# Kernel tuning notes

Measured on AMD Instinct MI355X. Metric: run time of the kernel, lower is better.

The kernel has to match this reference:

```python
import jax, jax.numpy as jnp
import numpy as np

EMBED_DIM = 128
BATCH = 8
SEQ = 2048


def setup_inputs() -> dict:
    key = jax.random.key(0)
    k1, k2, k3 = jax.random.split(key, 3)
    inputs = jax.random.normal(k1, (BATCH, SEQ, EMBED_DIM), dtype=jnp.float32)
    rotation_params = jax.random.normal(k2, (EMBED_DIM * 3,), dtype=jnp.float32)
    entangle_params = jax.random.normal(k3, (EMBED_DIM,), dtype=jnp.float32)
    return {"inputs": inputs, "rotation_params": rotation_params, "entangle_params": entangle_params}


def reference(inputs, rotation_params, entangle_params):
    d = inputs.shape[-1]
    rot = rotation_params.reshape(d, 3)          # [d, 3]
    ent = entangle_params.reshape(d, 1)          # [d, 1]
    query = inputs @ rot                         # [B, S, 3]
    key = inputs @ ent                           # [B, S, 1]
    # scores: [B, S, S], softmax over last axis
    logits = jnp.einsum('bsk,btk->bst', query, key) / jnp.sqrt(jnp.float32(d))
    scores = jax.nn.softmax(logits, axis=-1)
    return jnp.einsum('bst,btd->bsd', scores, inputs)  # [B, S, d]
```

## Files before the change

kernel.cpp:

```cpp
#include <hip/hip_runtime.h>
#include <cstddef>
#include <cstdint>

#define SS 2048
#define DD 128
#define NB 8

typedef _Float16 half8 __attribute__((ext_vector_type(8)));
typedef __attribute__((ext_vector_type(16))) float f32x16;

#define WS_A2   0
#define WS_KV   (NB*SS*4)
#define WS_XF   (2*NB*SS*4)
#define BATCH_B (SS*DD*2)
#define WS_NEED (size_t)(WS_XF + (size_t)NB*BATCH_B)
#define WS_KMX  (WS_XF)
#define WS_KMN  (WS_XF + 128)


__global__ __launch_bounds__(256) void prep(
    const float* __restrict__ X, const float* __restrict__ rotp,
    const float* __restrict__ entp, uint8_t* __restrict__ ws, int do_x) {
  __shared__ __align__(16) uint8_t lbuf[128 * 80];
  const int blk = blockIdx.x;
  const int b = blk & 7;
  const int rc = blk >> 3;
  const int tid = threadIdx.x;
  const int d4 = (tid & 31) * 4;
  float* a2out = (float*)(ws + WS_A2);
  float* kout = (float*)(ws + WS_KV);

  const float4 f0 = *reinterpret_cast<const float4*>(rotp + d4 * 3);
  const float4 f1 = *reinterpret_cast<const float4*>(rotp + d4 * 3 + 4);
  const float4 f2 = *reinterpret_cast<const float4*>(rotp + d4 * 3 + 8);
  const float rs0 = f0.x + f0.y + f0.z;
  const float rs1 = f0.w + f1.x + f1.y;
  const float rs2 = f1.z + f1.w + f2.x;
  const float rs3 = f2.y + f2.z + f2.w;
  const float4 e4 = *reinterpret_cast<const float4*>(entp + d4);

#pragma unroll
  for (int rnd = 0; rnd < 4; ++rnd) {
    const int t31 = rnd * 8 + (tid >> 5);
    const int tg = rc * 32 + t31;
    const float4 xv =
        *reinterpret_cast<const float4*>(X + ((size_t)b * SS + tg) * DD + d4);
    float av = xv.x * rs0 + xv.y * rs1 + xv.z * rs2 + xv.w * rs3;
    float kv = xv.x * e4.x + xv.y * e4.y + xv.z * e4.z + xv.w * e4.w;
#pragma unroll
    for (int off = 16; off > 0; off >>= 1) {
      av += __shfl_xor(av, off, 64);
      kv += __shfl_xor(kv, off, 64);
    }
    if ((tid & 31) == 0) {
      a2out[b * SS + tg] = av * (0.08838834764831845f * 1.4426950408889634f);
      kout[b * SS + tg] = kv;
    }
    if (do_x) {
      const float vv[4] = {xv.x, xv.y, xv.z, xv.w};
#pragma unroll
      for (int i = 0; i < 4; ++i)
        *reinterpret_cast<_Float16*>(lbuf + (d4 + i) * 80 + t31 * 2) =
            (_Float16)vv[i];
    }
  }

  if (do_x) {
    __syncthreads();
    const int T = rc >> 2;
    const int wfb = (rc & 3) * 2;
    uint8_t* outb = ws + WS_XF + (size_t)b * BATCH_B + (T * 8 + wfb) * 4096;
    const int nt = tid >> 6;
    const int lane = tid & 63;
    const int hh = lane >> 5;
    const int d = nt * 32 + (lane & 31);
#pragma unroll
    for (int wfl = 0; wfl < 2; ++wfl) {
      const half8 v = *reinterpret_cast<const half8*>(
          lbuf + d * 80 + (wfl * 16 + hh * 8) * 2);
      *reinterpret_cast<half8*>(outb + wfl * 4096 + nt * 1024 + lane * 16) = v;
    }
  }
}

__global__ __launch_bounds__(512, 2) void attn_mfma(
    const uint8_t* __restrict__ ws, float* __restrict__ out) {
  __shared__ float comb[2][64 * 128];
  __shared__ float dl[8 * 64];
  __shared__ float smx[8], smn[8];
  const int tid = threadIdx.x;
  const int w = tid >> 6;
  const int lane = tid & 63;
  const int lm = lane & 31;
  const int h = lane >> 5;
  const int blk = blockIdx.x;
  const int b = blk & 7;
  const int s0 = (blk >> 3) * 64;

  const float* a2 = (const float*)(ws + WS_A2) + b * SS;
  const float* kb = (const float*)(ws + WS_KV) + b * SS;
  const uint8_t* xf = ws + WS_XF + (size_t)b * BATCH_B;

  const float4 k4 = *reinterpret_cast<const float4*>(kb + tid * 4);
  float mx = fmaxf(fmaxf(k4.x, k4.y), fmaxf(k4.z, k4.w));
  float mn = fminf(fminf(k4.x, k4.y), fminf(k4.z, k4.w));
#pragma unroll
  for (int off = 32; off > 0; off >>= 1) {
    mx = fmaxf(mx, __shfl_xor(mx, off, 64));
    mn = fminf(mn, __shfl_xor(mn, off, 64));
  }
  if (lane == 0) { smx[w] = mx; smn[w] = mn; }
  const float ga0 = a2[s0 + lm];
  const float ga1 = a2[s0 + 32 + lm];
  __syncthreads();
  mx = smx[0]; mn = smn[0];
#pragma unroll
  for (int q = 1; q < 8; ++q) { mx = fmaxf(mx, smx[q]); mn = fminf(mn, smn[q]); }
  const float gm0 = fmaxf(ga0 * mx, ga0 * mn);
  const float gm1 = fmaxf(ga1 * mx, ga1 * mn);
  float gden0 = 0.0f, gden1 = 0.0f;

  f32x16 acc0[4], acc1[4];
#pragma unroll
  for (int nt = 0; nt < 4; ++nt)
#pragma unroll
    for (int r = 0; r < 16; ++r) { acc0[nt][r] = 0.0f; acc1[nt][r] = 0.0f; }

  const uint8_t* wb = xf + w * 4096 + lane * 16;
  half8 bf[4];
#pragma unroll
  for (int nt = 0; nt < 4; ++nt)
    bf[nt] = *reinterpret_cast<const half8*>(wb + nt * 1024);

  for (int T = 0; T < 16; ++T) {
    half8 bn[4];
    if (T < 15) {
      const uint8_t* nb_ = wb + (T + 1) * 32768;
#pragma unroll
      for (int nt = 0; nt < 4; ++nt)
        bn[nt] = *reinterpret_cast<const half8*>(nb_ + nt * 1024);
    }
    const float* kp = kb + T * 128 + w * 16 + h * 8;
    const float4 ka = *reinterpret_cast<const float4*>(kp);
    const float4 kc = *reinterpret_cast<const float4*>(kp + 4);
    const float kv8[8] = {ka.x, ka.y, ka.z, ka.w, kc.x, kc.y, kc.z, kc.w};
    half8 wa0, wa1;
#pragma unroll
    for (int j = 0; j < 8; ++j) {
      const float v0 = exp2f(fmaf(ga0, kv8[j], -gm0));
      const float v1 = exp2f(fmaf(ga1, kv8[j], -gm1));
      gden0 += v0; gden1 += v1;
      wa0[j] = (_Float16)v0;
      wa1[j] = (_Float16)v1;
    }
    __builtin_amdgcn_s_setprio(1);
#pragma unroll
    for (int nt = 0; nt < 4; ++nt) {
      acc0[nt] = __builtin_amdgcn_mfma_f32_32x32x16_f16(wa0, bf[nt], acc0[nt], 0, 0, 0);
      acc1[nt] = __builtin_amdgcn_mfma_f32_32x32x16_f16(wa1, bf[nt], acc1[nt], 0, 0, 0);
    }
    __builtin_amdgcn_s_setprio(0);
#pragma unroll
    for (int nt = 0; nt < 4; ++nt) bf[nt] = bn[nt];
  }

  gden0 += __shfl_xor(gden0, 32, 64);
  gden1 += __shfl_xor(gden1, 32, 64);
  if (lane < 32) { dl[w * 64 + lane] = gden0; dl[w * 64 + 32 + lane] = gden1; }
#pragma unroll
  for (int p = 0; p < 4; ++p) {
    const int grp = w >> 2;
    if ((w & 3) == p) {
      float* cb = comb[grp];
#pragma unroll
      for (int nt = 0; nt < 4; ++nt)
#pragma unroll
        for (int r = 0; r < 16; ++r) {
          const int rr = (r & 3) + 8 * (r >> 2) + 4 * h;
          const int i0 = rr * 128 + nt * 32 + lm;
          const int i1 = (32 + rr) * 128 + nt * 32 + lm;
          if (p == 0) { cb[i0] = acc0[nt][r]; cb[i1] = acc1[nt][r]; }
          else        { cb[i0] += acc0[nt][r]; cb[i1] += acc1[nt][r]; }
        }
    }
    __syncthreads();
  }

  const int r = tid >> 3;
  const int cg = (tid & 7) * 16;
  float den = 0.0f;
#pragma unroll
  for (int q = 0; q < 8; ++q) den += dl[q * 64 + r];
  const float inv = 1.0f / den;
  float* orow = out + ((size_t)b * SS + s0 + r) * DD + cg;
#pragma unroll
  for (int q = 0; q < 4; ++q) {
    const float4 vA = *reinterpret_cast<const float4*>(&comb[0][r * 128 + cg + q * 4]);
    const float4 vB = *reinterpret_cast<const float4*>(&comb[1][r * 128 + cg + q * 4]);
    *reinterpret_cast<float4*>(orow + q * 4) =
        make_float4((vA.x + vB.x) * inv, (vA.y + vB.y) * inv,
                    (vA.z + vB.z) * inv, (vA.w + vB.w) * inv);
  }
}

__global__ __launch_bounds__(256) void kminmax(const float* __restrict__ kvec,
                                               float* __restrict__ kmx,
                                               float* __restrict__ kmn) {
  const int b = blockIdx.x;
  const int tid = threadIdx.x;
  float mx = -1e30f, mn = 1e30f;
  for (int i = tid; i < SS; i += 256) {
    const float v = kvec[b * SS + i];
    mx = fmaxf(mx, v);
    mn = fminf(mn, v);
  }
#pragma unroll
  for (int off = 32; off > 0; off >>= 1) {
    mx = fmaxf(mx, __shfl_xor(mx, off, 64));
    mn = fminf(mn, __shfl_xor(mn, off, 64));
  }
  __shared__ float smx[4], smn[4];
  const int wid = tid >> 6, lane = tid & 63;
  if (lane == 0) { smx[wid] = mx; smn[wid] = mn; }
  __syncthreads();
  if (tid == 0) {
    kmx[b] = fmaxf(fmaxf(smx[0], smx[1]), fmaxf(smx[2], smx[3]));
    kmn[b] = fminf(fminf(smn[0], smn[1]), fminf(smn[2], smn[3]));
  }
}

__global__ __launch_bounds__(256) void attn_main(
    const float* __restrict__ X, const float* __restrict__ a2,
    const float* __restrict__ kvec, const float* __restrict__ kmx,
    const float* __restrict__ kmn, float* __restrict__ out) {
  __shared__ float xs[64 * DD];
  __shared__ float wt[64 * 32];
  __shared__ float denp[8 * 32];
  const int tid = threadIdx.x;
  const int tx = tid & 15;
  const int ty = (tid >> 4) & 3;
  const int tz = tid >> 6;
  const int b = blockIdx.y;
  const int s0 = blockIdx.x * 32;
  const int sg = tid & 31;
  const int tq = tid >> 5;
  const float ga = a2[b * SS + s0 + sg];
  const float gm = fmaxf(ga * kmx[b], ga * kmn[b]);
  float gden = 0.0f;
  float acc[8][8];
#pragma unroll
  for (int r = 0; r < 8; ++r)
#pragma unroll
    for (int c = 0; c < 8; ++c) acc[r][c] = 0.0f;
  const float* xb = X + (size_t)b * SS * DD;
  const float* kb = kvec + b * SS;
  for (int t0 = 0; t0 < SS; t0 += 64) {
    __syncthreads();
#pragma unroll
    for (int rnd = 0; rnd < 8; ++rnd) {
      const int idx = rnd * 1024 + tid * 4;
      *reinterpret_cast<float4*>(xs + idx) =
          *reinterpret_cast<const float4*>(xb + t0 * DD + idx);
    }
#pragma unroll
    for (int j = 0; j < 8; ++j) {
      const float kt = kb[t0 + tq * 8 + j];
      const float wv = exp2f(fmaf(ga, kt, -gm));
      wt[(tq * 8 + j) * 32 + sg] = wv;
      gden += wv;
    }
    __syncthreads();
#pragma unroll 4
    for (int ti = 0; ti < 16; ++ti) {
      const int tl = tz * 16 + ti;
      const float4 x0 = *reinterpret_cast<const float4*>(xs + tl * DD + tx * 8);
      const float4 x1 = *reinterpret_cast<const float4*>(xs + tl * DD + tx * 8 + 4);
      const float4 w0 = *reinterpret_cast<const float4*>(wt + tl * 32 + ty * 8);
      const float4 w1 = *reinterpret_cast<const float4*>(wt + tl * 32 + ty * 8 + 4);
      const float xr[8] = {x0.x, x0.y, x0.z, x0.w, x1.x, x1.y, x1.z, x1.w};
      const float wr[8] = {w0.x, w0.y, w0.z, w0.w, w1.x, w1.y, w1.z, w1.w};
#pragma unroll
      for (int r = 0; r < 8; ++r)
#pragma unroll
        for (int c = 0; c < 8; ++c) acc[r][c] = fmaf(wr[r], xr[c], acc[r][c]);
    }
  }
  __syncthreads();
  denp[tq * 32 + sg] = gden;
  for (int p = 1; p < 4; ++p) {
    __syncthreads();
    if (tz == p) {
#pragma unroll
      for (int r = 0; r < 8; ++r) {
        const int sl = ty * 8 + r;
        *reinterpret_cast<float4*>(xs + sl * DD + tx * 8) =
            make_float4(acc[r][0], acc[r][1], acc[r][2], acc[r][3]);
        *reinterpret_cast<float4*>(xs + sl * DD + tx * 8 + 4) =
            make_float4(acc[r][4], acc[r][5], acc[r][6], acc[r][7]);
      }
    }
    __syncthreads();
    if (tz == 0) {
#pragma unroll
      for (int r = 0; r < 8; ++r) {
        const int sl = ty * 8 + r;
        const float4 v0 = *reinterpret_cast<const float4*>(xs + sl * DD + tx * 8);
        const float4 v1 = *reinterpret_cast<const float4*>(xs + sl * DD + tx * 8 + 4);
        acc[r][0] += v0.x; acc[r][1] += v0.y; acc[r][2] += v0.z; acc[r][3] += v0.w;
        acc[r][4] += v1.x; acc[r][5] += v1.y; acc[r][6] += v1.z; acc[r][7] += v1.w;
      }
    }
  }
  if (tz == 0) {
#pragma unroll
    for (int r = 0; r < 8; ++r) {
      const int sl = ty * 8 + r;
      float den = 0.0f;
#pragma unroll
      for (int q = 0; q < 8; ++q) den += denp[q * 32 + sl];
      const float inv = 1.0f / den;
      float* orow = out + ((size_t)b * SS + s0 + sl) * DD + tx * 8;
      *reinterpret_cast<float4*>(orow) =
          make_float4(acc[r][0] * inv, acc[r][1] * inv, acc[r][2] * inv, acc[r][3] * inv);
      *reinterpret_cast<float4*>(orow + 4) =
          make_float4(acc[r][4] * inv, acc[r][5] * inv, acc[r][6] * inv, acc[r][7] * inv);
    }
  }
}

extern "C" void kernel_launch(void* const* d_in, const int* in_sizes, int n_in,
                              void* d_out, int out_size, void* d_ws, size_t ws_size,
                              hipStream_t stream) {
  const float* X = (const float*)d_in[0];
  const float* rotp = (const float*)d_in[1];
  const float* entp = (const float*)d_in[2];
  float* out = (float*)d_out;
  uint8_t* ws = (uint8_t*)d_ws;

  if (ws_size >= WS_NEED) {
    prep<<<512, 256, 0, stream>>>(X, rotp, entp, ws, 1);
    attn_mfma<<<256, 512, 0, stream>>>((const uint8_t*)ws, out);
  } else {
    float* a2 = (float*)(ws + WS_A2);
    float* kv = (float*)(ws + WS_KV);
    float* kmxp = (float*)(ws + WS_KMX);
    float* kmnp = (float*)(ws + WS_KMN);
    prep<<<512, 256, 0, stream>>>(X, rotp, entp, ws, 0);
    kminmax<<<NB, 256, 0, stream>>>(kv, kmxp, kmnp);
    attn_main<<<dim3(SS / 32, NB), 256, 0, stream>>>(X, a2, kv, kmxp, kmnp, out);
  }
}
```

Baseline: 31.62 us.

## Halve query rows per block to double grid size and occupancy

Each attention block now handles 32 query rows instead of 64, so the grid doubles to 512 blocks and launch bounds allow 4 blocks per CU. Shared memory and accumulator registers are halved to fit. The exponential uses the hardware exp2 builtin, and the fp16 conversion uses packed round-toward-zero conversion. The aim is to fill all 256 CUs and cheapen the per-element softmax math, at the cost of loading each X tile twice as many times across blocks.

```diff
diff --git a/kernel.cpp b/kernel.cpp
--- a/kernel.cpp
+++ b/kernel.cpp
@@ -7,7 +7,14 @@
 #define NB 8
 
 typedef _Float16 half8 __attribute__((ext_vector_type(8)));
+typedef __fp16 fp16x2 __attribute__((ext_vector_type(2)));
 typedef __attribute__((ext_vector_type(16))) float f32x16;
+
+#if __has_builtin(__builtin_amdgcn_exp2f)
+#define EXP2F(x) __builtin_amdgcn_exp2f(x)
+#else
+#define EXP2F(x) exp2f(x)
+#endif
 
 #define WS_A2   0
 #define WS_KV   (NB*SS*4)
@@ -83,10 +90,10 @@
   }
 }
 
-__global__ __launch_bounds__(512, 2) void attn_mfma(
+__global__ __launch_bounds__(512, 4) void attn_mfma(
     const uint8_t* __restrict__ ws, float* __restrict__ out) {
-  __shared__ float comb[2][64 * 128];
-  __shared__ float dl[8 * 64];
+  __shared__ float comb[2][32 * 128];
+  __shared__ float dl[8 * 32];
   __shared__ float smx[8], smn[8];
   const int tid = threadIdx.x;
   const int w = tid >> 6;
@@ -95,7 +102,7 @@
   const int h = lane >> 5;
   const int blk = blockIdx.x;
   const int b = blk & 7;
-  const int s0 = (blk >> 3) * 64;
+  const int s0 = (blk >> 3) * 32;
 
   const float* a2 = (const float*)(ws + WS_A2) + b * SS;
   const float* kb = (const float*)(ws + WS_KV) + b * SS;
@@ -110,23 +117,23 @@
     mn = fminf(mn, __shfl_xor(mn, off, 64));
   }
   if (lane == 0) { smx[w] = mx; smn[w] = mn; }
-  const float ga0 = a2[s0 + lm];
-  const float ga1 = a2[s0 + 32 + lm];
+  const float ga = a2[s0 + lm];
   __syncthreads();
   mx = smx[0]; mn = smn[0];
 #pragma unroll
   for (int q = 1; q < 8; ++q) { mx = fmaxf(mx, smx[q]); mn = fminf(mn, smn[q]); }
-  const float gm0 = fmaxf(ga0 * mx, ga0 * mn);
-  const float gm1 = fmaxf(ga1 * mx, ga1 * mn);
-  float gden0 = 0.0f, gden1 = 0.0f;
-
-  f32x16 acc0[4], acc1[4];
+  const float gm = fmaxf(ga * mx, ga * mn);
+  float gden = 0.0f;
+
+  f32x16 acc[4];
 #pragma unroll
   for (int nt = 0; nt < 4; ++nt)
 #pragma unroll
-    for (int r = 0; r < 16; ++r) { acc0[nt][r] = 0.0f; acc1[nt][r] = 0.0f; }
+    for (int r = 0; r < 16; ++r) acc[nt][r] = 0.0f;
 
   const uint8_t* wb = xf + w * 4096 + lane * 16;
+  const float* kp0 = kb + w * 16 + h * 8;
+
   half8 bf[4];
 #pragma unroll
   for (int nt = 0; nt < 4; ++nt)
@@ -140,33 +147,31 @@
       for (int nt = 0; nt < 4; ++nt)
         bn[nt] = *reinterpret_cast<const half8*>(nb_ + nt * 1024);
     }
-    const float* kp = kb + T * 128 + w * 16 + h * 8;
+    const float* kp = kp0 + T * 128;
     const float4 ka = *reinterpret_cast<const float4*>(kp);
     const float4 kc = *reinterpret_cast<const float4*>(kp + 4);
     const float kv8[8] = {ka.x, ka.y, ka.z, ka.w, kc.x, kc.y, kc.z, kc.w};
-    half8 wa0, wa1;
+    float e0[8];
 #pragma unroll
     for (int j = 0; j < 8; ++j) {
-      const float v0 = exp2f(fmaf(ga0, kv8[j], -gm0));
-      const float v1 = exp2f(fmaf(ga1, kv8[j], -gm1));
-      gden0 += v0; gden1 += v1;
-      wa0[j] = (_Float16)v0;
-      wa1[j] = (_Float16)v1;
-    }
+      e0[j] = EXP2F(fmaf(ga, kv8[j], -gm));
+      gden += e0[j];
+    }
+    union { half8 v; fp16x2 p[4]; } wa;
+#pragma unroll
+    for (int q = 0; q < 4; ++q)
+      wa.p[q] = __builtin_amdgcn_cvt_pkrtz(e0[2 * q], e0[2 * q + 1]);
     __builtin_amdgcn_s_setprio(1);
 #pragma unroll
-    for (int nt = 0; nt < 4; ++nt) {
-      acc0[nt] = __builtin_amdgcn_mfma_f32_32x32x16_f16(wa0, bf[nt], acc0[nt], 0, 0, 0);
-      acc1[nt] = __builtin_amdgcn_mfma_f32_32x32x16_f16(wa1, bf[nt], acc1[nt], 0, 0, 0);
-    }
+    for (int nt = 0; nt < 4; ++nt)
+      acc[nt] = __builtin_amdgcn_mfma_f32_32x32x16_f16(wa.v, bf[nt], acc[nt], 0, 0, 0);
     __builtin_amdgcn_s_setprio(0);
 #pragma unroll
     for (int nt = 0; nt < 4; ++nt) bf[nt] = bn[nt];
   }
 
-  gden0 += __shfl_xor(gden0, 32, 64);
-  gden1 += __shfl_xor(gden1, 32, 64);
-  if (lane < 32) { dl[w * 64 + lane] = gden0; dl[w * 64 + 32 + lane] = gden1; }
+  gden += __shfl_xor(gden, 32, 64);
+  if (lane < 32) dl[w * 32 + lane] = gden;
 #pragma unroll
   for (int p = 0; p < 4; ++p) {
     const int grp = w >> 2;
@@ -178,23 +183,22 @@
         for (int r = 0; r < 16; ++r) {
           const int rr = (r & 3) + 8 * (r >> 2) + 4 * h;
           const int i0 = rr * 128 + nt * 32 + lm;
-          const int i1 = (32 + rr) * 128 + nt * 32 + lm;
-          if (p == 0) { cb[i0] = acc0[nt][r]; cb[i1] = acc1[nt][r]; }
-          else        { cb[i0] += acc0[nt][r]; cb[i1] += acc1[nt][r]; }
+          if (p == 0) cb[i0] = acc[nt][r];
+          else        cb[i0] += acc[nt][r];
         }
     }
     __syncthreads();
   }
 
-  const int r = tid >> 3;
-  const int cg = (tid & 7) * 16;
+  const int r = tid >> 4;
+  const int cg = (tid & 15) * 8;
   float den = 0.0f;
 #pragma unroll
-  for (int q = 0; q < 8; ++q) den += dl[q * 64 + r];
+  for (int q = 0; q < 8; ++q) den += dl[q * 32 + r];
   const float inv = 1.0f / den;
   float* orow = out + ((size_t)b * SS + s0 + r) * DD + cg;
 #pragma unroll
-  for (int q = 0; q < 4; ++q) {
+  for (int q = 0; q < 2; ++q) {
     const float4 vA = *reinterpret_cast<const float4*>(&comb[0][r * 128 + cg + q * 4]);
     const float4 vB = *reinterpret_cast<const float4*>(&comb[1][r * 128 + cg + q * 4]);
     *reinterpret_cast<float4*>(orow + q * 4) =
@@ -339,7 +343,7 @@
 
   if (ws_size >= WS_NEED) {
     prep<<<512, 256, 0, stream>>>(X, rotp, entp, ws, 1);
-    attn_mfma<<<256, 512, 0, stream>>>((const uint8_t*)ws, out);
+    attn_mfma<<<512, 512, 0, stream>>>((const uint8_t*)ws, out);
   } else {
     float* a2 = (float*)(ws + WS_A2);
     float* kv = (float*)(ws + WS_KV);
```

New measurement: 28.46 us. 1.11x faster.
